# Performance work log

Hardware: AMD Instinct MI355X
Metric: run time of the kernel (lower is better)

The kernel has to match this reference:

```python
import jax, jax.numpy as jnp
import numpy as np

B, S, D, H, F = 2, 4096, 768, 12, 3072
DK = D // H
EPS = 1e-6


def _ln(x, g, b):
    mu = jnp.mean(x, axis=-1, keepdims=True)
    var = jnp.mean(jnp.square(x - mu), axis=-1, keepdims=True)
    return (x - mu) * jax.lax.rsqrt(var + EPS) * g + b


def setup_inputs() -> dict:
    key = jax.random.key(0)
    ks = jax.random.split(key, 12)
    sc = 0.02
    inp = {
        "inputs_q": jax.random.normal(ks[0], (B, S, D), jnp.float32),
        "inputs_k": jax.random.normal(ks[1], (B, S, D), jnp.float32),
        "inputs_v": jax.random.normal(ks[2], (B, S, D), jnp.float32),
        "mask": jnp.ones((B, 1, 1, S), jnp.int32),
        "wq": jax.random.normal(ks[3], (D, D), jnp.float32) * sc,
        "bq": jnp.zeros((D,), jnp.float32),
        "wk": jax.random.normal(ks[4], (D, D), jnp.float32) * sc,
        "bk": jnp.zeros((D,), jnp.float32),
        "wv": jax.random.normal(ks[5], (D, D), jnp.float32) * sc,
        "bv": jnp.zeros((D,), jnp.float32),
        "wo": jax.random.normal(ks[6], (D, D), jnp.float32) * sc,
        "bo": jnp.zeros((D,), jnp.float32),
        "w1": jax.random.normal(ks[7], (D, F), jnp.float32) * sc,
        "b1": jnp.zeros((F,), jnp.float32),
        "w2": jax.random.normal(ks[8], (F, D), jnp.float32) * sc,
        "b2": jnp.zeros((D,), jnp.float32),
        "g1": jnp.ones((D,), jnp.float32),
        "be1": jnp.zeros((D,), jnp.float32),
        "g2": jnp.ones((D,), jnp.float32),
        "be2": jnp.zeros((D,), jnp.float32),
    }
    return inp


def reference(inputs_q, inputs_k, inputs_v, mask, wq, bq, wk, bk, wv, bv,
              wo, bo, w1, b1, w2, b2, g1, be1, g2, be2):
    # --- multi-head self-attention (naive, unfused as in source) ---
    q = (inputs_q @ wq + bq).reshape(B, S, H, DK).transpose(0, 2, 1, 3)  # [B,H,S,DK]
    k = (inputs_k @ wk + bk).reshape(B, S, H, DK).transpose(0, 2, 1, 3)
    v = (inputs_v @ wv + bv).reshape(B, S, H, DK).transpose(0, 2, 1, 3)
    scores = jnp.einsum("bhqd,bhkd->bhqk", q, k) / np.sqrt(DK)  # [B,H,S,S]
    scores = jnp.where(mask == 0, -jnp.inf, scores)
    attn = jax.nn.softmax(scores, axis=-1)
    ctx = jnp.einsum("bhqk,bhkd->bhqd", attn, v)
    ctx = ctx.transpose(0, 2, 1, 3).reshape(B, S, D)
    attn_out = ctx @ wo + bo
    # --- residual + LN, FFN, residual + LN (dropout p=0 -> identity) ---
    x1 = _ln(inputs_q + attn_out, g1, be1)
    ffn = jax.nn.relu(x1 @ w1 + b1) @ w2 + b2
    return _ln(x1 + ffn, g2, be2)
```

## Files before the change

### kernel.cpp

```cpp
#include <hip/hip_runtime.h>
#include <stdint.h>

#define B_ 2
#define S_ 4096
#define D_ 768
#define H_ 12
#define F_ 3072
#define DK_ 64
#define QBLK 128
#define KVB 64
#define NT (S_ / KVB)

typedef __bf16 bf16x8 __attribute__((ext_vector_type(8)));
typedef float floatx4 __attribute__((ext_vector_type(4)));
typedef float floatx16 __attribute__((ext_vector_type(16)));

__device__ __forceinline__ float bf2f(unsigned short u) {
  unsigned int x = ((unsigned int)u) << 16;
  return __builtin_bit_cast(float, x);
}
__device__ __forceinline__ unsigned short f2bf(float f) {
  unsigned int x = __builtin_bit_cast(unsigned int, f);
  x += 0x7FFFu + ((x >> 16) & 1u);
  return (unsigned short)(x >> 16);
}
__device__ __forceinline__ unsigned int cvtpk_bf16(float lo, float hi) {
  unsigned int r;
  asm("v_cvt_pk_bf16_f32 %0, %1, %2" : "=v"(r) : "v"(lo), "v"(hi));
  return r;
}

__device__ __forceinline__ void wtrans_core(const float* __restrict__ w,
                                            unsigned short* __restrict__ wt,
                                            int K, int N) {
  __shared__ float tile[32][33];
  const int n0 = blockIdx.x * 32, k0 = blockIdx.y * 32;
  const int tx = threadIdx.x & 31, ty8 = threadIdx.x >> 5;
#pragma unroll
  for (int r = 0; r < 4; r++)
    tile[ty8 + r * 8][tx] = w[(size_t)(k0 + ty8 + r * 8) * N + n0 + tx];
  __syncthreads();
#pragma unroll
  for (int r = 0; r < 4; r++)
    wt[(size_t)(n0 + ty8 + r * 8) * K + k0 + tx] = f2bf(tile[tx][ty8 + r * 8]);
}

__global__ __launch_bounds__(256) void wtrans(const float* __restrict__ w,
                                              unsigned short* __restrict__ wt,
                                              int K, int N) {
  wtrans_core(w, wt, K, N);
}

__global__ __launch_bounds__(256) void wtrans4(const float* __restrict__ w0,
                                               const float* __restrict__ w1,
                                               const float* __restrict__ w2,
                                               const float* __restrict__ w3,
                                               unsigned short* __restrict__ wtbase) {
  const int z = blockIdx.z;
  const float* w = (z == 0) ? w0 : (z == 1) ? w1 : (z == 2) ? w2 : w3;
  wtrans_core(w, wtbase + (size_t)z * 589824, 768, 768);
}

__global__ __launch_bounds__(256) void cvt_bf16_3(const float* __restrict__ x0,
                                                  const float* __restrict__ x1,
                                                  const float* __restrict__ x2,
                                                  unsigned short* __restrict__ ybase, int n8) {
  const int z = blockIdx.z;
  const float* x = (z == 0) ? x0 : (z == 1) ? x1 : x2;
  unsigned short* y = ybase + (size_t)z * 6291456;
  const int i = blockIdx.x * 256 + threadIdx.x;
  if (i >= n8) return;
  const float4 a = ((const float4*)x)[2 * i];
  const float4 b = ((const float4*)x)[2 * i + 1];
  uint4 o;
  o.x = (unsigned int)f2bf(a.x) | ((unsigned int)f2bf(a.y) << 16);
  o.y = (unsigned int)f2bf(a.z) | ((unsigned int)f2bf(a.w) << 16);
  o.z = (unsigned int)f2bf(b.x) | ((unsigned int)f2bf(b.y) << 16);
  o.w = (unsigned int)f2bf(b.z) | ((unsigned int)f2bf(b.w) << 16);
  ((uint4*)y)[i] = o;
}

template <bool RELU, int RESID_MODE, bool OUT_BF16>
__device__ __forceinline__ void gemm_core(
    const unsigned short* __restrict__ A, const unsigned short* __restrict__ Bt,
    const float* __restrict__ bias, const void* __restrict__ residv,
    void* __restrict__ outv, unsigned short* __restrict__ vtout,
    float oscale, int M, int N, int K) {
  __shared__ __align__(16) unsigned short As[128 * 64];
  __shared__ __align__(16) unsigned short Bs[128 * 64];
  int bx = blockIdx.x, by = blockIdx.y;
  {
    const int gx = gridDim.x;
    const int nwg = gx * gridDim.y;
    const int flat = by * gx + bx;
    const int wg = (flat & 7) * (nwg >> 3) + (flat >> 3);
    bx = wg % gx; by = wg / gx;
  }
  const int t = threadIdx.x;
  const int lane = t & 63, wave = t >> 6;
  const int m0 = by * 128, n0 = bx * 128;
  const int wm = (wave >> 1) * 64, wn = (wave & 1) * 64;
  const int rl = lane & 15, kl = (lane >> 4) * 8;
  const int lrow = lane >> 3, lcol = (lane & 7) * 8;

  floatx4 zf = {0.f, 0.f, 0.f, 0.f};
  floatx4 acc[4][4];
#pragma unroll
  for (int i = 0; i < 4; i++)
#pragma unroll
    for (int j = 0; j < 4; j++) acc[i][j] = zf;

  const unsigned short* Ab = A + (size_t)(m0 + wave * 32 + lrow) * K + lcol;
  const unsigned short* Bb = Bt + (size_t)(n0 + wave * 32 + lrow) * K + lcol;
  unsigned short* AsW = As + wave * 2048;
  unsigned short* BsW = Bs + wave * 2048;

  for (int k0 = 0; k0 < K; k0 += 64) {
    __syncthreads();
#pragma unroll
    for (int ld = 0; ld < 4; ld++) {
      __builtin_amdgcn_global_load_lds(Ab + k0 + (size_t)(ld * 8) * K, AsW + ld * 512, 16, 0, 0);
      __builtin_amdgcn_global_load_lds(Bb + k0 + (size_t)(ld * 8) * K, BsW + ld * 512, 16, 0, 0);
    }
    __syncthreads();
#pragma unroll
    for (int ks = 0; ks < 2; ks++) {
      bf16x8 af[4], bff[4];
#pragma unroll
      for (int i = 0; i < 4; i++)
        af[i] = __builtin_bit_cast(bf16x8, *(const uint4*)&As[(wm + i * 16 + rl) * 64 + ks * 32 + kl]);
#pragma unroll
      for (int j = 0; j < 4; j++)
        bff[j] = __builtin_bit_cast(bf16x8, *(const uint4*)&Bs[(wn + j * 16 + rl) * 64 + ks * 32 + kl]);
#pragma unroll
      for (int i = 0; i < 4; i++)
#pragma unroll
        for (int j = 0; j < 4; j++)
          acc[i][j] = __builtin_amdgcn_mfma_f32_16x16x32_bf16(af[i], bff[j], acc[i][j], 0, 0, 0);
    }
  }

  const int r0 = (lane >> 4) * 4;
  if (vtout) {
#pragma unroll
    for (int i = 0; i < 4; i++) {
#pragma unroll
      for (int j = 0; j < 4; j++) {
        const int col = n0 + wn + j * 16 + rl;
        const float bv = bias[col];
        const int rowb = m0 + wm + i * 16 + r0;
        const int bb = rowb >> 12, s = rowb & 4095;
        unsigned short e[4];
#pragma unroll
        for (int r = 0; r < 4; r++) e[r] = f2bf(acc[i][j][r] + bv);
        *(uint2*)&vtout[((size_t)bb * D_ + col) * 4096 + s] =
            make_uint2((unsigned int)e[0] | ((unsigned int)e[1] << 16),
                       (unsigned int)e[2] | ((unsigned int)e[3] << 16));
      }
    }
    return;
  }
#pragma unroll
  for (int i = 0; i < 4; i++) {
#pragma unroll
    for (int j = 0; j < 4; j++) {
      const int col = n0 + wn + j * 16 + rl;
      const float bv = bias[col];
#pragma unroll
      for (int r = 0; r < 4; r++) {
        const int row = m0 + wm + i * 16 + r0 + r;
        float v = (acc[i][j][r] + bv) * oscale;
        if (RESID_MODE == 1) v += ((const float*)residv)[(size_t)row * N + col];
        if (RESID_MODE == 2) v += bf2f(((const unsigned short*)residv)[(size_t)row * N + col]);
        if (RELU) v = v > 0.f ? v : 0.f;
        if (OUT_BF16)
          ((unsigned short*)outv)[(size_t)row * N + col] = f2bf(v);
        else
          ((float*)outv)[(size_t)row * N + col] = v;
      }
    }
  }
}

template <bool RELU, int RESID_MODE, bool OUT_BF16>
__global__ __launch_bounds__(256, 3) void gemm_lds(
    const unsigned short* __restrict__ A, const unsigned short* __restrict__ Bt,
    const float* __restrict__ bias, const void* __restrict__ residv,
    void* __restrict__ outv, int M, int N, int K) {
  gemm_core<RELU, RESID_MODE, OUT_BF16>(A, Bt, bias, residv, outv, nullptr, 1.0f, M, N, K);
}

__global__ __launch_bounds__(256, 3) void gemm_qkv(
    const unsigned short* __restrict__ Abase, const unsigned short* __restrict__ Btbase,
    const float* __restrict__ b0, const float* __restrict__ b1, const float* __restrict__ b2,
    unsigned short* __restrict__ outbase, unsigned short* __restrict__ vtb) {
  const int z = blockIdx.z;
  const float* bp = (z == 0) ? b0 : (z == 1) ? b1 : b2;
  const float sc = (z == 0) ? 0.180336880111120419f : 1.0f;
  gemm_core<false, 0, true>(Abase + (size_t)z * 6291456, Btbase + (size_t)z * 589824,
                            bp, nullptr, outbase + (size_t)z * 6291456,
                            (z == 2) ? vtb : nullptr, sc, 8192, 768, 768);
}

__global__ __launch_bounds__(256, 3) void flash_attn_v7(
    const unsigned short* __restrict__ qg, const unsigned short* __restrict__ kg,
    const unsigned short* __restrict__ vtg, const int* __restrict__ maskg,
    unsigned short* __restrict__ ctx) {
  __shared__ __align__(16) unsigned short Ks[2][64][64];
  __shared__ __align__(16) unsigned short Vt[2][64][64];
  __shared__ unsigned char TFlag[NT];

  const int t = threadIdx.x;
  const int L = t & 63, wv = t >> 6;
  const int q5 = L & 31, h5 = L >> 5;
  const int qb = blockIdx.x, h = blockIdx.y, b = blockIdx.z;
  const size_t bS = (size_t)b * S_;
  const int hb = h * DK_;
  const unsigned short* kbase = kg + bS * D_ + hb;
  const int* mp = maskg + bS;

  for (int tt = wv; tt < NT; tt += 4) {
    const int mv = mp[tt * KVB + L];
    const unsigned long long bal = __ballot(mv != 0);
    if (L == 0) TFlag[tt] = (bal == ~0ull) ? 1 : 0;
  }

  bf16x8 bq[4];
  {
    const unsigned short* qp = qg + (bS + qb * QBLK + wv * 32 + q5) * D_ + hb + h5 * 8;
#pragma unroll
    for (int ks = 0; ks < 4; ks++)
      bq[ks] = __builtin_bit_cast(bf16x8, *(const uint4*)(qp + ks * 16));
  }

  floatx16 o0, o1;
#pragma unroll
  for (int r = 0; r < 16; r++) { o0[r] = 0.f; o1[r] = 0.f; }
  float l_ = 0.f;

  const int srow = t >> 2, kc = (t & 3) * 2;
  const unsigned short* vtbase = vtg + ((size_t)b * D_ + hb + srow) * 4096;
  const int cshift = q5 & 7;

  uint4 kr0, kr1, vr0, vr1;
  {
    const unsigned short* kp = kbase + (size_t)srow * D_ + kc * 8;
    kr0 = *(const uint4*)kp; kr1 = *(const uint4*)(kp + 8);
    vr0 = *(const uint4*)(vtbase + kc * 8); vr1 = *(const uint4*)(vtbase + kc * 8 + 8);
    *(uint4*)&Ks[0][srow][((kc) ^ (srow & 7)) * 8] = kr0;
    *(uint4*)&Ks[0][srow][((kc + 1) ^ (srow & 7)) * 8] = kr1;
    *(uint4*)&Vt[0][srow][((kc) ^ (srow & 7)) * 8] = vr0;
    *(uint4*)&Vt[0][srow][((kc + 1) ^ (srow & 7)) * 8] = vr1;
  }
  __syncthreads();

  for (int kt = 0; kt < NT; kt++) {
    const int cur = kt & 1;
    const int kv0 = kt * KVB;
    if (kt + 1 < NT) {
      const unsigned short* kp = kbase + (size_t)(kv0 + KVB + srow) * D_ + kc * 8;
      kr0 = *(const uint4*)kp; kr1 = *(const uint4*)(kp + 8);
      vr0 = *(const uint4*)(vtbase + kv0 + KVB + kc * 8);
      vr1 = *(const uint4*)(vtbase + kv0 + KVB + kc * 8 + 8);
    }

    floatx16 s0, s1;
#pragma unroll
    for (int r = 0; r < 16; r++) { s0[r] = 0.f; s1[r] = 0.f; }
    __builtin_amdgcn_s_setprio(1);
#pragma unroll
    for (int ks = 0; ks < 4; ks++) {
      bf16x8 ak0 = __builtin_bit_cast(bf16x8, *(const uint4*)&Ks[cur][q5][(((ks << 1) | h5) ^ cshift) * 8]);
      bf16x8 ak1 = __builtin_bit_cast(bf16x8, *(const uint4*)&Ks[cur][32 + q5][(((ks << 1) | h5) ^ cshift) * 8]);
      s0 = __builtin_amdgcn_mfma_f32_32x32x16_bf16(ak0, bq[ks], s0, 0, 0, 0);
      s1 = __builtin_amdgcn_mfma_f32_32x32x16_bf16(ak1, bq[ks], s1, 0, 0, 0);
    }
    __builtin_amdgcn_s_setprio(0);

    if (TFlag[kt]) {
#pragma unroll
      for (int r = 0; r < 16; r++) {
        s0[r] = fminf(s0[r], 88.f);
        s1[r] = fminf(s1[r], 88.f);
      }
    } else {
#pragma unroll
      for (int r = 0; r < 16; r++) {
        const int kvl = (r & 3) + 8 * (r >> 2) + 4 * h5;
        s0[r] = fminf(s0[r] + (mp[kv0 + kvl] ? 0.f : -1e30f), 88.f);
        s1[r] = fminf(s1[r] + (mp[kv0 + 32 + kvl] ? 0.f : -1e30f), 88.f);
      }
    }
#pragma unroll
    for (int r = 0; r < 16; r++) {
      s0[r] = exp2f(s0[r]);
      s1[r] = exp2f(s1[r]);
    }
    float a8[8];
#pragma unroll
    for (int i = 0; i < 8; i++) a8[i] = (s0[i] + s0[i + 8]) + (s1[i] + s1[i + 8]);
    float lsum = ((a8[0] + a8[1]) + (a8[2] + a8[3])) + ((a8[4] + a8[5]) + (a8[6] + a8[7]));
    lsum += __shfl_xor(lsum, 32, 64);
    l_ += lsum;

    unsigned int w[16];
#pragma unroll
    for (int a = 0; a < 8; a++) {
      w[a] = cvtpk_bf16(s0[2 * a], s0[2 * a + 1]);
      w[8 + a] = cvtpk_bf16(s1[2 * a], s1[2 * a + 1]);
    }
#pragma unroll
    for (int ks = 0; ks < 4; ks++) {
      asm("v_permlane32_swap_b32 %0, %1" : "+v"(w[4 * ks]), "+v"(w[4 * ks + 2]));
      asm("v_permlane32_swap_b32 %0, %1" : "+v"(w[4 * ks + 1]), "+v"(w[4 * ks + 3]));
    }

    __builtin_amdgcn_s_setprio(1);
#pragma unroll
    for (int ks = 0; ks < 4; ks++) {
      const bf16x8 pa = __builtin_bit_cast(bf16x8,
          make_uint4(w[4 * ks], w[4 * ks + 1], w[4 * ks + 2], w[4 * ks + 3]));
      bf16x8 av0 = __builtin_bit_cast(bf16x8, *(const uint4*)&Vt[cur][q5][(((ks << 1) | h5) ^ cshift) * 8]);
      bf16x8 av1 = __builtin_bit_cast(bf16x8, *(const uint4*)&Vt[cur][32 + q5][(((ks << 1) | h5) ^ cshift) * 8]);
      o0 = __builtin_amdgcn_mfma_f32_32x32x16_bf16(av0, pa, o0, 0, 0, 0);
      o1 = __builtin_amdgcn_mfma_f32_32x32x16_bf16(av1, pa, o1, 0, 0, 0);
    }
    __builtin_amdgcn_s_setprio(0);

    if (kt + 1 < NT) {
      *(uint4*)&Ks[cur ^ 1][srow][((kc) ^ (srow & 7)) * 8] = kr0;
      *(uint4*)&Ks[cur ^ 1][srow][((kc + 1) ^ (srow & 7)) * 8] = kr1;
      *(uint4*)&Vt[cur ^ 1][srow][((kc) ^ (srow & 7)) * 8] = vr0;
      *(uint4*)&Vt[cur ^ 1][srow][((kc + 1) ^ (srow & 7)) * 8] = vr1;
    }
    __syncthreads();
  }

  {
    const float inv = 1.f / l_;
    unsigned int ep[16];
#pragma unroll
    for (int a = 0; a < 8; a++) {
      ep[a] = cvtpk_bf16(o0[2 * a] * inv, o0[2 * a + 1] * inv);
      ep[8 + a] = cvtpk_bf16(o1[2 * a] * inv, o1[2 * a + 1] * inv);
    }
    unsigned short* crow = ctx + (bS + qb * QBLK + wv * 32 + q5) * D_ + hb;
#pragma unroll
    for (int dt = 0; dt < 2; dt++)
#pragma unroll
      for (int g4 = 0; g4 < 4; g4++)
        *(uint2*)(crow + dt * 32 + g4 * 8 + h5 * 4) =
            make_uint2(ep[dt * 8 + g4 * 2], ep[dt * 8 + g4 * 2 + 1]);
  }
}

template <bool OUT_BF16>
__global__ __launch_bounds__(256) void ln_kernel(const float* __restrict__ x,
                                                 const float* __restrict__ g,
                                                 const float* __restrict__ be,
                                                 void* __restrict__ outv) {
  __shared__ float red[4];
  const int t = threadIdx.x, lane = t & 63, wave = t >> 6;
  const size_t row = blockIdx.x;
  const float* xr = x + row * D_;
  float v0 = xr[t], v1 = xr[t + 256], v2 = xr[t + 512];
  float s = v0 + v1 + v2;
#pragma unroll
  for (int off = 32; off; off >>= 1) s += __shfl_xor(s, off, 64);
  if (lane == 0) red[wave] = s;
  __syncthreads();
  const float mu = (red[0] + red[1] + red[2] + red[3]) * (1.f / 768.f);
  __syncthreads();
  const float d0 = v0 - mu, d1 = v1 - mu, d2 = v2 - mu;
  float vs = d0 * d0 + d1 * d1 + d2 * d2;
#pragma unroll
  for (int off = 32; off; off >>= 1) vs += __shfl_xor(vs, off, 64);
  if (lane == 0) red[wave] = vs;
  __syncthreads();
  const float rs = rsqrtf((red[0] + red[1] + red[2] + red[3]) * (1.f / 768.f) + 1e-6f);
  const float r0v = d0 * rs * g[t] + be[t];
  const float r1v = d1 * rs * g[t + 256] + be[t + 256];
  const float r2v = d2 * rs * g[t + 512] + be[t + 512];
  if (OUT_BF16) {
    unsigned short* o = (unsigned short*)outv + row * D_;
    o[t] = f2bf(r0v); o[t + 256] = f2bf(r1v); o[t + 512] = f2bf(r2v);
  } else {
    float* o = (float*)outv + row * D_;
    o[t] = r0v; o[t + 256] = r1v; o[t + 512] = r2v;
  }
}

extern "C" void kernel_launch(void* const* d_in, const int* in_sizes, int n_in,
                              void* d_out, int out_size, void* d_ws, size_t ws_size,
                              hipStream_t stream) {
  const float* xq = (const float*)d_in[0];
  const float* xk = (const float*)d_in[1];
  const float* xv = (const float*)d_in[2];
  const int* mask = (const int*)d_in[3];
  const float* wq = (const float*)d_in[4];
  const float* bq = (const float*)d_in[5];
  const float* wk = (const float*)d_in[6];
  const float* bk = (const float*)d_in[7];
  const float* wv = (const float*)d_in[8];
  const float* bv = (const float*)d_in[9];
  const float* wo = (const float*)d_in[10];
  const float* bo = (const float*)d_in[11];
  const float* w1 = (const float*)d_in[12];
  const float* b1 = (const float*)d_in[13];
  const float* w2 = (const float*)d_in[14];
  const float* b2 = (const float*)d_in[15];
  const float* g1 = (const float*)d_in[16];
  const float* be1 = (const float*)d_in[17];
  const float* g2 = (const float*)d_in[18];
  const float* be2 = (const float*)d_in[19];
  float* out = (float*)d_out;
  char* ws = (char*)d_ws;

  unsigned short* WQT = (unsigned short*)(ws + 0);
  unsigned short* W1T = (unsigned short*)(ws + 4718592);
  unsigned short* W2T = (unsigned short*)(ws + 9437184);
  unsigned short* XQB = (unsigned short*)(ws + 14155776);
  unsigned short* QB = (unsigned short*)(ws + 51904512);
  unsigned short* VTB = (unsigned short*)(ws + 77070336);
  unsigned short* CTXB = (unsigned short*)(ws + 14155776);
  float* X1PRE = (float*)(ws + 51904512);
  unsigned short* X1B = (unsigned short*)(ws + 77070336);
  unsigned short* HB = (unsigned short*)(ws + 14155776);
  float* X2PRE = (float*)(ws + 89653248);
  unsigned short* WOT = WQT + 3 * 589824;

  wtrans4<<<dim3(24, 24, 4), 256, 0, stream>>>(wq, wk, wv, wo, WQT);
  wtrans<<<dim3(96, 24), 256, 0, stream>>>(w1, W1T, 768, 3072);
  wtrans<<<dim3(24, 96), 256, 0, stream>>>(w2, W2T, 3072, 768);

  cvt_bf16_3<<<dim3(3072, 1, 3), 256, 0, stream>>>(xq, xk, xv, XQB, 786432);

  gemm_qkv<<<dim3(6, 64, 3), 256, 0, stream>>>(XQB, WQT, bq, bk, bv, QB, VTB);

  flash_attn_v7<<<dim3(S_ / QBLK, H_, B_), 256, 0, stream>>>(QB, QB + 6291456, VTB, mask, CTXB);

  gemm_lds<false, 1, false><<<dim3(6, 64), 256, 0, stream>>>(CTXB, WOT, bo, xq, X1PRE, 8192, 768, 768);

  ln_kernel<true><<<8192, 256, 0, stream>>>(X1PRE, g1, be1, X1B);

  gemm_lds<true, 0, true><<<dim3(24, 64), 256, 0, stream>>>(X1B, W1T, b1, nullptr, HB, 8192, 3072, 768);

  gemm_lds<false, 2, false><<<dim3(6, 64), 256, 0, stream>>>(HB, W2T, b2, X1B, X2PRE, 8192, 768, 3072);

  ln_kernel<false><<<8192, 256, 0, stream>>>(X2PRE, g2, be2, out);
}
```

Measured before the change: 408.3 us.

## Split each KV tile across two wave groups in flash attention

Flash attention now runs 512 threads per block, with 8 waves instead of 4. Each group of four waves covers the same 128 query rows but handles half of every 64-key tile, so each wave issues half as many score and PV MFMAs per tile. At the end the second group writes its partial output accumulators and row sums to shared memory, and the first group adds them before normalizing. The aim is to double the waves per block and hide latency better, at the cost of an extra reduction through LDS, another barrier, and more shared memory reuse. The softmax has no running max, so the partial sums can be added directly.

```diff
diff --git a/kernel.cpp b/kernel.cpp
--- a/kernel.cpp
+++ b/kernel.cpp
@@ -202,24 +202,27 @@
                             (z == 2) ? vtb : nullptr, sc, 8192, 768, 768);
 }
 
-__global__ __launch_bounds__(256, 3) void flash_attn_v7(
+__global__ __launch_bounds__(512, 6) void flash_attn_v8(
     const unsigned short* __restrict__ qg, const unsigned short* __restrict__ kg,
     const unsigned short* __restrict__ vtg, const int* __restrict__ maskg,
     unsigned short* __restrict__ ctx) {
-  __shared__ __align__(16) unsigned short Ks[2][64][64];
-  __shared__ __align__(16) unsigned short Vt[2][64][64];
-  __shared__ unsigned char TFlag[NT];
+  __shared__ __align__(16) unsigned char smem[33856];
+  unsigned short (*Ks)[64][64] = (unsigned short (*)[64][64])(smem);
+  unsigned short (*Vt)[64][64] = (unsigned short (*)[64][64])(smem + 16384);
+  unsigned char* TFlag = smem + 32768;
+  float* Lp = (float*)(smem + 32832);
 
   const int t = threadIdx.x;
   const int L = t & 63, wv = t >> 6;
   const int q5 = L & 31, h5 = L >> 5;
+  const int qgp = wv & 3, kvh = wv >> 2;
   const int qb = blockIdx.x, h = blockIdx.y, b = blockIdx.z;
   const size_t bS = (size_t)b * S_;
   const int hb = h * DK_;
   const unsigned short* kbase = kg + bS * D_ + hb;
   const int* mp = maskg + bS;
 
-  for (int tt = wv; tt < NT; tt += 4) {
+  for (int tt = wv; tt < NT; tt += 8) {
     const int mv = mp[tt * KVB + L];
     const unsigned long long bal = __ballot(mv != 0);
     if (L == 0) TFlag[tt] = (bal == ~0ull) ? 1 : 0;
@@ -227,7 +230,7 @@
 
   bf16x8 bq[4];
   {
-    const unsigned short* qp = qg + (bS + qb * QBLK + wv * 32 + q5) * D_ + hb + h5 * 8;
+    const unsigned short* qp = qg + (bS + qb * QBLK + qgp * 32 + q5) * D_ + hb + h5 * 8;
 #pragma unroll
     for (int ks = 0; ks < 4; ks++)
       bq[ks] = __builtin_bit_cast(bf16x8, *(const uint4*)(qp + ks * 16));
@@ -238,19 +241,17 @@
   for (int r = 0; r < 16; r++) { o0[r] = 0.f; o1[r] = 0.f; }
   float l_ = 0.f;
 
-  const int srow = t >> 2, kc = (t & 3) * 2;
+  const int srow = t >> 3, kc = t & 7;
   const unsigned short* vtbase = vtg + ((size_t)b * D_ + hb + srow) * 4096;
   const int cshift = q5 & 7;
-
-  uint4 kr0, kr1, vr0, vr1;
+  const int krow = 32 * kvh + q5;
+
+  uint4 kr, vr;
   {
-    const unsigned short* kp = kbase + (size_t)srow * D_ + kc * 8;
-    kr0 = *(const uint4*)kp; kr1 = *(const uint4*)(kp + 8);
-    vr0 = *(const uint4*)(vtbase + kc * 8); vr1 = *(const uint4*)(vtbase + kc * 8 + 8);
-    *(uint4*)&Ks[0][srow][((kc) ^ (srow & 7)) * 8] = kr0;
-    *(uint4*)&Ks[0][srow][((kc + 1) ^ (srow & 7)) * 8] = kr1;
-    *(uint4*)&Vt[0][srow][((kc) ^ (srow & 7)) * 8] = vr0;
-    *(uint4*)&Vt[0][srow][((kc + 1) ^ (srow & 7)) * 8] = vr1;
+    kr = *(const uint4*)(kbase + (size_t)srow * D_ + kc * 8);
+    vr = *(const uint4*)(vtbase + kc * 8);
+    *(uint4*)&Ks[0][srow][(kc ^ (srow & 7)) * 8] = kr;
+    *(uint4*)&Vt[0][srow][(kc ^ (srow & 7)) * 8] = vr;
   }
   __syncthreads();
 
@@ -258,93 +259,99 @@
     const int cur = kt & 1;
     const int kv0 = kt * KVB;
     if (kt + 1 < NT) {
-      const unsigned short* kp = kbase + (size_t)(kv0 + KVB + srow) * D_ + kc * 8;
-      kr0 = *(const uint4*)kp; kr1 = *(const uint4*)(kp + 8);
-      vr0 = *(const uint4*)(vtbase + kv0 + KVB + kc * 8);
-      vr1 = *(const uint4*)(vtbase + kv0 + KVB + kc * 8 + 8);
-    }
-
-    floatx16 s0, s1;
-#pragma unroll
-    for (int r = 0; r < 16; r++) { s0[r] = 0.f; s1[r] = 0.f; }
+      kr = *(const uint4*)(kbase + (size_t)(kv0 + KVB + srow) * D_ + kc * 8);
+      vr = *(const uint4*)(vtbase + kv0 + KVB + kc * 8);
+    }
+
+    floatx16 s;
+#pragma unroll
+    for (int r = 0; r < 16; r++) s[r] = 0.f;
     __builtin_amdgcn_s_setprio(1);
 #pragma unroll
     for (int ks = 0; ks < 4; ks++) {
-      bf16x8 ak0 = __builtin_bit_cast(bf16x8, *(const uint4*)&Ks[cur][q5][(((ks << 1) | h5) ^ cshift) * 8]);
-      bf16x8 ak1 = __builtin_bit_cast(bf16x8, *(const uint4*)&Ks[cur][32 + q5][(((ks << 1) | h5) ^ cshift) * 8]);
-      s0 = __builtin_amdgcn_mfma_f32_32x32x16_bf16(ak0, bq[ks], s0, 0, 0, 0);
-      s1 = __builtin_amdgcn_mfma_f32_32x32x16_bf16(ak1, bq[ks], s1, 0, 0, 0);
+      bf16x8 ak = __builtin_bit_cast(bf16x8,
+          *(const uint4*)&Ks[cur][krow][(((ks << 1) | h5) ^ cshift) * 8]);
+      s = __builtin_amdgcn_mfma_f32_32x32x16_bf16(ak, bq[ks], s, 0, 0, 0);
     }
     __builtin_amdgcn_s_setprio(0);
 
     if (TFlag[kt]) {
 #pragma unroll
+      for (int r = 0; r < 16; r++) s[r] = fminf(s[r], 88.f);
+    } else {
+#pragma unroll
       for (int r = 0; r < 16; r++) {
-        s0[r] = fminf(s0[r], 88.f);
-        s1[r] = fminf(s1[r], 88.f);
+        const int kvl = 32 * kvh + (r & 3) + 8 * (r >> 2) + 4 * h5;
+        s[r] = fminf(s[r] + (mp[kv0 + kvl] ? 0.f : -1e30f), 88.f);
       }
-    } else {
-#pragma unroll
-      for (int r = 0; r < 16; r++) {
-        const int kvl = (r & 3) + 8 * (r >> 2) + 4 * h5;
-        s0[r] = fminf(s0[r] + (mp[kv0 + kvl] ? 0.f : -1e30f), 88.f);
-        s1[r] = fminf(s1[r] + (mp[kv0 + 32 + kvl] ? 0.f : -1e30f), 88.f);
-      }
-    }
-#pragma unroll
-    for (int r = 0; r < 16; r++) {
-      s0[r] = exp2f(s0[r]);
-      s1[r] = exp2f(s1[r]);
-    }
-    float a8[8];
-#pragma unroll
-    for (int i = 0; i < 8; i++) a8[i] = (s0[i] + s0[i + 8]) + (s1[i] + s1[i + 8]);
-    float lsum = ((a8[0] + a8[1]) + (a8[2] + a8[3])) + ((a8[4] + a8[5]) + (a8[6] + a8[7]));
+    }
+#pragma unroll
+    for (int r = 0; r < 16; r++) s[r] = exp2f(s[r]);
+
+    float a4[4];
+#pragma unroll
+    for (int i = 0; i < 4; i++) a4[i] = (s[i] + s[i + 4]) + (s[i + 8] + s[i + 12]);
+    float lsum = (a4[0] + a4[1]) + (a4[2] + a4[3]);
     lsum += __shfl_xor(lsum, 32, 64);
     l_ += lsum;
 
-    unsigned int w[16];
-#pragma unroll
-    for (int a = 0; a < 8; a++) {
-      w[a] = cvtpk_bf16(s0[2 * a], s0[2 * a + 1]);
-      w[8 + a] = cvtpk_bf16(s1[2 * a], s1[2 * a + 1]);
-    }
-#pragma unroll
-    for (int ks = 0; ks < 4; ks++) {
-      asm("v_permlane32_swap_b32 %0, %1" : "+v"(w[4 * ks]), "+v"(w[4 * ks + 2]));
-      asm("v_permlane32_swap_b32 %0, %1" : "+v"(w[4 * ks + 1]), "+v"(w[4 * ks + 3]));
+    unsigned int w[8];
+#pragma unroll
+    for (int a = 0; a < 8; a++) w[a] = cvtpk_bf16(s[2 * a], s[2 * a + 1]);
+#pragma unroll
+    for (int g = 0; g < 2; g++) {
+      asm("v_permlane32_swap_b32 %0, %1" : "+v"(w[4 * g]), "+v"(w[4 * g + 2]));
+      asm("v_permlane32_swap_b32 %0, %1" : "+v"(w[4 * g + 1]), "+v"(w[4 * g + 3]));
     }
 
     __builtin_amdgcn_s_setprio(1);
 #pragma unroll
-    for (int ks = 0; ks < 4; ks++) {
+    for (int g = 0; g < 2; g++) {
+      const int ksg = 2 * kvh + g;
       const bf16x8 pa = __builtin_bit_cast(bf16x8,
-          make_uint4(w[4 * ks], w[4 * ks + 1], w[4 * ks + 2], w[4 * ks + 3]));
-      bf16x8 av0 = __builtin_bit_cast(bf16x8, *(const uint4*)&Vt[cur][q5][(((ks << 1) | h5) ^ cshift) * 8]);
-      bf16x8 av1 = __builtin_bit_cast(bf16x8, *(const uint4*)&Vt[cur][32 + q5][(((ks << 1) | h5) ^ cshift) * 8]);
+          make_uint4(w[4 * g], w[4 * g + 1], w[4 * g + 2], w[4 * g + 3]));
+      bf16x8 av0 = __builtin_bit_cast(bf16x8,
+          *(const uint4*)&Vt[cur][q5][(((ksg << 1) | h5) ^ cshift) * 8]);
+      bf16x8 av1 = __builtin_bit_cast(bf16x8,
+          *(const uint4*)&Vt[cur][32 + q5][(((ksg << 1) | h5) ^ cshift) * 8]);
       o0 = __builtin_amdgcn_mfma_f32_32x32x16_bf16(av0, pa, o0, 0, 0, 0);
       o1 = __builtin_amdgcn_mfma_f32_32x32x16_bf16(av1, pa, o1, 0, 0, 0);
     }
     __builtin_amdgcn_s_setprio(0);
 
     if (kt + 1 < NT) {
-      *(uint4*)&Ks[cur ^ 1][srow][((kc) ^ (srow & 7)) * 8] = kr0;
-      *(uint4*)&Ks[cur ^ 1][srow][((kc + 1) ^ (srow & 7)) * 8] = kr1;
-      *(uint4*)&Vt[cur ^ 1][srow][((kc) ^ (srow & 7)) * 8] = vr0;
-      *(uint4*)&Vt[cur ^ 1][srow][((kc + 1) ^ (srow & 7)) * 8] = vr1;
+      *(uint4*)&Ks[cur ^ 1][srow][(kc ^ (srow & 7)) * 8] = kr;
+      *(uint4*)&Vt[cur ^ 1][srow][(kc ^ (srow & 7)) * 8] = vr;
     }
     __syncthreads();
   }
 
-  {
-    const float inv = 1.f / l_;
+  float2* Op = (float2*)smem;
+  if (kvh == 1) {
+#pragma unroll
+    for (int i = 0; i < 8; i++) {
+      Op[(qgp * 16 + i) * 64 + L] = make_float2(o0[2 * i], o0[2 * i + 1]);
+      Op[(qgp * 16 + 8 + i) * 64 + L] = make_float2(o1[2 * i], o1[2 * i + 1]);
+    }
+    Lp[qgp * 64 + L] = l_;
+  }
+  __syncthreads();
+  if (kvh == 0) {
+#pragma unroll
+    for (int i = 0; i < 8; i++) {
+      const float2 p0 = Op[(qgp * 16 + i) * 64 + L];
+      const float2 p1 = Op[(qgp * 16 + 8 + i) * 64 + L];
+      o0[2 * i] += p0.x; o0[2 * i + 1] += p0.y;
+      o1[2 * i] += p1.x; o1[2 * i + 1] += p1.y;
+    }
+    const float inv = 1.f / (l_ + Lp[qgp * 64 + L]);
     unsigned int ep[16];
 #pragma unroll
     for (int a = 0; a < 8; a++) {
       ep[a] = cvtpk_bf16(o0[2 * a] * inv, o0[2 * a + 1] * inv);
       ep[8 + a] = cvtpk_bf16(o1[2 * a] * inv, o1[2 * a + 1] * inv);
     }
-    unsigned short* crow = ctx + (bS + qb * QBLK + wv * 32 + q5) * D_ + hb;
+    unsigned short* crow = ctx + (bS + qb * QBLK + qgp * 32 + q5) * D_ + hb;
 #pragma unroll
     for (int dt = 0; dt < 2; dt++)
 #pragma unroll
@@ -437,7 +444,7 @@
 
   gemm_qkv<<<dim3(6, 64, 3), 256, 0, stream>>>(XQB, WQT, bq, bk, bv, QB, VTB);
 
-  flash_attn_v7<<<dim3(S_ / QBLK, H_, B_), 256, 0, stream>>>(QB, QB + 6291456, VTB, mask, CTXB);
+  flash_attn_v8<<<dim3(S_ / QBLK, H_, B_), 512, 0, stream>>>(QB, QB + 6291456, VTB, mask, CTXB);
 
   gemm_lds<false, 1, false><<<dim3(6, 64), 256, 0, stream>>>(CTXB, WOT, bo, xq, X1PRE, 8192, 768, 768);
 
```

After: 684.4 us. 67.6% more time.

## Split attention KV range into two halves and combine partial outputs

Applied to the files above, without the earlier changes.

The flash attention kernel now gives each grid block half of the KV tiles, doubling the block count to 1536. Each half writes unnormalized fp32 partial outputs and row sums to workspace. A new combine kernel adds the two partials, normalizes them and writes the bf16 context. The goal is more parallelism and better load balance across CUs. In exchange it adds fp32 partial-output traffic to memory and an extra kernel launch, and the workspace layout is reshuffled to make room.

```diff
diff --git a/kernel.cpp b/kernel.cpp
--- a/kernel.cpp
+++ b/kernel.cpp
@@ -202,10 +202,11 @@
                             (z == 2) ? vtb : nullptr, sc, 8192, 768, 768);
 }
 
-__global__ __launch_bounds__(256, 3) void flash_attn_v7(
+__global__ __launch_bounds__(256, 3) void flash_attn_v9(
     const unsigned short* __restrict__ qg, const unsigned short* __restrict__ kg,
     const unsigned short* __restrict__ vtg, const int* __restrict__ maskg,
-    unsigned short* __restrict__ ctx) {
+    float* __restrict__ po0, float* __restrict__ po1,
+    float* __restrict__ pl0, float* __restrict__ pl1) {
   __shared__ __align__(16) unsigned short Ks[2][64][64];
   __shared__ __align__(16) unsigned short Vt[2][64][64];
   __shared__ unsigned char TFlag[NT];
@@ -213,13 +214,15 @@
   const int t = threadIdx.x;
   const int L = t & 63, wv = t >> 6;
   const int q5 = L & 31, h5 = L >> 5;
-  const int qb = blockIdx.x, h = blockIdx.y, b = blockIdx.z;
+  const int qb = blockIdx.x, h = blockIdx.y;
+  const int b = blockIdx.z >> 1, half = blockIdx.z & 1;
+  const int ktbeg = half * (NT / 2), ktend = ktbeg + NT / 2;
   const size_t bS = (size_t)b * S_;
   const int hb = h * DK_;
   const unsigned short* kbase = kg + bS * D_ + hb;
   const int* mp = maskg + bS;
 
-  for (int tt = wv; tt < NT; tt += 4) {
+  for (int tt = ktbeg + wv; tt < ktend; tt += 4) {
     const int mv = mp[tt * KVB + L];
     const unsigned long long bal = __ballot(mv != 0);
     if (L == 0) TFlag[tt] = (bal == ~0ull) ? 1 : 0;
@@ -244,9 +247,10 @@
 
   uint4 kr0, kr1, vr0, vr1;
   {
-    const unsigned short* kp = kbase + (size_t)srow * D_ + kc * 8;
+    const unsigned short* kp = kbase + (size_t)(ktbeg * KVB + srow) * D_ + kc * 8;
     kr0 = *(const uint4*)kp; kr1 = *(const uint4*)(kp + 8);
-    vr0 = *(const uint4*)(vtbase + kc * 8); vr1 = *(const uint4*)(vtbase + kc * 8 + 8);
+    vr0 = *(const uint4*)(vtbase + ktbeg * KVB + kc * 8);
+    vr1 = *(const uint4*)(vtbase + ktbeg * KVB + kc * 8 + 8);
     *(uint4*)&Ks[0][srow][((kc) ^ (srow & 7)) * 8] = kr0;
     *(uint4*)&Ks[0][srow][((kc + 1) ^ (srow & 7)) * 8] = kr1;
     *(uint4*)&Vt[0][srow][((kc) ^ (srow & 7)) * 8] = vr0;
@@ -254,10 +258,10 @@
   }
   __syncthreads();
 
-  for (int kt = 0; kt < NT; kt++) {
+  for (int kt = ktbeg; kt < ktend; kt++) {
     const int cur = kt & 1;
     const int kv0 = kt * KVB;
-    if (kt + 1 < NT) {
+    if (kt + 1 < ktend) {
       const unsigned short* kp = kbase + (size_t)(kv0 + KVB + srow) * D_ + kc * 8;
       kr0 = *(const uint4*)kp; kr1 = *(const uint4*)(kp + 8);
       vr0 = *(const uint4*)(vtbase + kv0 + KVB + kc * 8);
@@ -327,7 +331,7 @@
     }
     __builtin_amdgcn_s_setprio(0);
 
-    if (kt + 1 < NT) {
+    if (kt + 1 < ktend) {
       *(uint4*)&Ks[cur ^ 1][srow][((kc) ^ (srow & 7)) * 8] = kr0;
       *(uint4*)&Ks[cur ^ 1][srow][((kc + 1) ^ (srow & 7)) * 8] = kr1;
       *(uint4*)&Vt[cur ^ 1][srow][((kc) ^ (srow & 7)) * 8] = vr0;
@@ -337,21 +341,37 @@
   }
 
   {
-    const float inv = 1.f / l_;
-    unsigned int ep[16];
-#pragma unroll
-    for (int a = 0; a < 8; a++) {
-      ep[a] = cvtpk_bf16(o0[2 * a] * inv, o0[2 * a + 1] * inv);
-      ep[8 + a] = cvtpk_bf16(o1[2 * a] * inv, o1[2 * a + 1] * inv);
-    }
-    unsigned short* crow = ctx + (bS + qb * QBLK + wv * 32 + q5) * D_ + hb;
-#pragma unroll
-    for (int dt = 0; dt < 2; dt++)
-#pragma unroll
-      for (int g4 = 0; g4 < 4; g4++)
-        *(uint2*)(crow + dt * 32 + g4 * 8 + h5 * 4) =
-            make_uint2(ep[dt * 8 + g4 * 2], ep[dt * 8 + g4 * 2 + 1]);
-  }
+    float* po = (half ? po1 : po0) + (bS + qb * QBLK + wv * 32 + q5) * (size_t)D_ + hb;
+#pragma unroll
+    for (int g4 = 0; g4 < 4; g4++) {
+      *(float4*)(po + g4 * 8 + h5 * 4) =
+          make_float4(o0[4 * g4], o0[4 * g4 + 1], o0[4 * g4 + 2], o0[4 * g4 + 3]);
+      *(float4*)(po + 32 + g4 * 8 + h5 * 4) =
+          make_float4(o1[4 * g4], o1[4 * g4 + 1], o1[4 * g4 + 2], o1[4 * g4 + 3]);
+    }
+    if (h5 == 0)
+      (half ? pl1 : pl0)[((size_t)(b * H_ + h) << 12) + qb * QBLK + wv * 32 + q5] = l_;
+  }
+}
+
+__global__ __launch_bounds__(256) void attn_combine(
+    const float* __restrict__ po0, const float* __restrict__ po1,
+    const float* __restrict__ pl0, const float* __restrict__ pl1,
+    unsigned short* __restrict__ ctx) {
+  const int gid = blockIdx.x * 256 + threadIdx.x;
+  const size_t e = (size_t)gid * 8;
+  const int row = (int)(e / D_), col = (int)(e % D_);
+  const int h = col >> 6, b = row >> 12, s = row & 4095;
+  const size_t li = ((size_t)(b * H_ + h) << 12) + s;
+  const float inv = 1.f / (pl0[li] + pl1[li]);
+  const float4 a0 = *(const float4*)(po0 + e), a1 = *(const float4*)(po0 + e + 4);
+  const float4 c0 = *(const float4*)(po1 + e), c1 = *(const float4*)(po1 + e + 4);
+  uint4 o;
+  o.x = cvtpk_bf16((a0.x + c0.x) * inv, (a0.y + c0.y) * inv);
+  o.y = cvtpk_bf16((a0.z + c0.z) * inv, (a0.w + c0.w) * inv);
+  o.z = cvtpk_bf16((a1.x + c1.x) * inv, (a1.y + c1.y) * inv);
+  o.w = cvtpk_bf16((a1.z + c1.z) * inv, (a1.w + c1.w) * inv);
+  *(uint4*)(ctx + e) = o;
 }
 
 template <bool OUT_BF16>
@@ -422,11 +442,15 @@
   unsigned short* XQB = (unsigned short*)(ws + 14155776);
   unsigned short* QB = (unsigned short*)(ws + 51904512);
   unsigned short* VTB = (unsigned short*)(ws + 77070336);
-  unsigned short* CTXB = (unsigned short*)(ws + 14155776);
-  float* X1PRE = (float*)(ws + 51904512);
-  unsigned short* X1B = (unsigned short*)(ws + 77070336);
-  unsigned short* HB = (unsigned short*)(ws + 14155776);
-  float* X2PRE = (float*)(ws + 89653248);
+  float* PO0 = (float*)(ws + 14155776);
+  float* PL0 = (float*)(ws + 39321600);
+  float* PL1 = (float*)(ws + 39714816);
+  float* PO1 = (float*)(ws + 89653248);
+  unsigned short* CTXB = (unsigned short*)(ws + 51904512);
+  float* X1PRE = (float*)(ws + 64487424);
+  unsigned short* X1B = (unsigned short*)(ws + 14155776);
+  unsigned short* HB = (unsigned short*)(ws + 26738688);
+  float* X2PRE = (float*)(ws + 77070336);
   unsigned short* WOT = WQT + 3 * 589824;
 
   wtrans4<<<dim3(24, 24, 4), 256, 0, stream>>>(wq, wk, wv, wo, WQT);
@@ -437,7 +461,10 @@
 
   gemm_qkv<<<dim3(6, 64, 3), 256, 0, stream>>>(XQB, WQT, bq, bk, bv, QB, VTB);
 
-  flash_attn_v7<<<dim3(S_ / QBLK, H_, B_), 256, 0, stream>>>(QB, QB + 6291456, VTB, mask, CTXB);
+  flash_attn_v9<<<dim3(S_ / QBLK, H_, B_ * 2), 256, 0, stream>>>(
+      QB, QB + 6291456, VTB, mask, PO0, PO1, PL0, PL1);
+
+  attn_combine<<<3072, 256, 0, stream>>>(PO0, PO1, PL0, PL1, CTXB);
 
   gemm_lds<false, 1, false><<<dim3(6, 64), 256, 0, stream>>>(CTXB, WOT, bo, xq, X1PRE, 8192, 768, 768);
 
```

Result: slower. 417.6 us (+2.3%).
